# Optimization experiments

Hardware: AMD Instinct MI355X
Metric: run time of the kernel (lower is better)

## Reference

```python
import jax, jax.numpy as jnp
import numpy as np


def setup_inputs() -> dict:
    key = jax.random.key(0)
    k1, k2, k3 = jax.random.split(key, 3)
    B, D, G = 128, 1024, 40
    x = jax.random.normal(k1, (B, D), dtype=jnp.float32)
    g = jax.random.randint(k2, (B,), 0, 100, dtype=jnp.int64)
    layer_transform_0 = jax.random.normal(k3, (G, D, D), dtype=jnp.float32)
    return {"x": x, "g": g, "layer_transform_0": layer_transform_0, "l": 0, "n": 1}


def reference(x, g, layer_transform_0, l, n):
    # l selects which layer transform table; only one table here (layer_sizes=[1024]).
    # n is unused by the original forward.
    G = layer_transform_0.shape[0]
    shape = x.shape
    xf = x.reshape(shape[0], -1)               # (B, D)
    idx = g % G                                 # (B,)
    T = layer_transform_0[idx]                  # (B, D, D) gathered per-sample matrices
    out = jnp.einsum('bd,bde->be', xf, T)       # batched matvec (M=1 bmm)
    return out.reshape(shape)
```

## Files before the change

kernel.cpp:

```cpp
#include <hip/hip_runtime.h>


#define B_DIM   128
#define D_DIM   1024
#define G_DIM   40
#define DSPLIT  16
#define DCHUNK  (D_DIM / DSPLIT)
#define SMAX    8
#define THREADS 256

template <int USE_ATOMIC>
__global__ __launch_bounds__(THREADS) void leqfc_grouped(
    const float* __restrict__ x,
    const int* __restrict__ g,
    const float* __restrict__ T,
    float* __restrict__ part,
    float* __restrict__ out)
{
    const int gi  = blockIdx.x;
    const int dc  = blockIdx.y;
    const int dbase = dc * DCHUNK;
    const int tid = threadIdx.x;

    __shared__ int   mem[B_DIM];
    __shared__ int   cnt;
    __shared__ float xs[SMAX][DCHUNK];

    if (tid == 0) cnt = 0;
    __syncthreads();
    if (tid < B_DIM) {
        if ((g[tid] % G_DIM) == gi) {
            int i = atomicAdd(&cnt, 1);
            mem[i] = tid;
        }
    }
    __syncthreads();
    const int m = cnt;

    const float* __restrict__ Tg = T + (size_t)gi * D_DIM * D_DIM;
    const float4* __restrict__ Trow =
        reinterpret_cast<const float4*>(Tg + (size_t)dbase * D_DIM) + tid;

    for (int s0 = 0; s0 < m; s0 += SMAX) {
        const int mc = min(SMAX, m - s0);

        __syncthreads();
        #pragma unroll
        for (int k = 0; k < (SMAX * DCHUNK) / THREADS; ++k) {
            int idx = tid + k * THREADS;
            int j  = idx >> 6;
            int dd = idx & (DCHUNK - 1);
            xs[j][dd] = (j < mc)
                ? x[(size_t)mem[s0 + j] * D_DIM + dbase + dd]
                : 0.0f;
        }
        __syncthreads();

        float4 acc[SMAX];
        #pragma unroll
        for (int j = 0; j < SMAX; ++j) acc[j] = make_float4(0.f, 0.f, 0.f, 0.f);

        #pragma unroll 4
        for (int dd = 0; dd < DCHUNK; ++dd) {
            float4 t = Trow[(size_t)dd * (D_DIM / 4)];
            #pragma unroll
            for (int j = 0; j < SMAX; ++j) {
                float xv = xs[j][dd];
                acc[j].x = fmaf(xv, t.x, acc[j].x);
                acc[j].y = fmaf(xv, t.y, acc[j].y);
                acc[j].z = fmaf(xv, t.z, acc[j].z);
                acc[j].w = fmaf(xv, t.w, acc[j].w);
            }
        }

        #pragma unroll
        for (int j = 0; j < SMAX; ++j) {
            if (j < mc) {
                const int b = mem[s0 + j];
                if (USE_ATOMIC) {
                    float* o = out + (size_t)b * D_DIM + tid * 4;
                    atomicAdd(o + 0, acc[j].x);
                    atomicAdd(o + 1, acc[j].y);
                    atomicAdd(o + 2, acc[j].z);
                    atomicAdd(o + 3, acc[j].w);
                } else {
                    float4* o = reinterpret_cast<float4*>(
                        part + ((size_t)dc * B_DIM + b) * D_DIM) + tid;
                    *o = acc[j];
                }
            }
        }
    }
}

__global__ __launch_bounds__(256) void leqfc_reduce(
    const float* __restrict__ part, float* __restrict__ out)
{
    const int idx = blockIdx.x * 256 + threadIdx.x;
    float s = 0.f;
    #pragma unroll
    for (int p = 0; p < DSPLIT; ++p)
        s += part[(size_t)p * B_DIM * D_DIM + idx];
    out[idx] = s;
}

__global__ __launch_bounds__(256) void leqfc_zero(float* __restrict__ out)
{
    out[blockIdx.x * 256 + threadIdx.x] = 0.f;
}

extern "C" void kernel_launch(void* const* d_in, const int* in_sizes, int n_in,
                              void* d_out, int out_size, void* d_ws, size_t ws_size,
                              hipStream_t stream)
{
    const float* x = (const float*)d_in[0];
    const int*   g = (const int*)d_in[1];
    const float* T = (const float*)d_in[2];
    float* out = (float*)d_out;

    const size_t need = (size_t)DSPLIT * B_DIM * D_DIM * sizeof(float);
    dim3 grid(G_DIM, DSPLIT);

    if (ws_size >= need) {
        float* part = (float*)d_ws;
        leqfc_grouped<0><<<grid, THREADS, 0, stream>>>(x, g, T, part, nullptr);
        leqfc_reduce<<<(B_DIM * D_DIM) / 256, 256, 0, stream>>>(part, out);
    } else {
        leqfc_zero<<<(B_DIM * D_DIM) / 256, 256, 0, stream>>>(out);
        leqfc_grouped<1><<<grid, THREADS, 0, stream>>>(x, g, T, nullptr, out);
    }
}
```

Before: 33.40 us.

## Double the D split, prefetch T rows into registers, vectorize the reduction

```diff
diff --git a/kernel.cpp b/kernel.cpp
--- a/kernel.cpp
+++ b/kernel.cpp
@@ -4,10 +4,11 @@
 #define B_DIM   128
 #define D_DIM   1024
 #define G_DIM   40
-#define DSPLIT  16
+#define DSPLIT  32
 #define DCHUNK  (D_DIM / DSPLIT)
 #define SMAX    8
 #define THREADS 256
+#define PF      8
 
 template <int USE_ATOMIC>
 __global__ __launch_bounds__(THREADS) void leqfc_grouped(
@@ -17,10 +18,10 @@
     float* __restrict__ part,
     float* __restrict__ out)
 {
-    const int gi  = blockIdx.x;
-    const int dc  = blockIdx.y;
+    const int gi    = blockIdx.x;
+    const int dc    = blockIdx.y;
     const int dbase = dc * DCHUNK;
-    const int tid = threadIdx.x;
+    const int tid   = threadIdx.x;
 
     __shared__ int   mem[B_DIM];
     __shared__ int   cnt;
@@ -45,11 +46,9 @@
         const int mc = min(SMAX, m - s0);
 
         __syncthreads();
-        #pragma unroll
-        for (int k = 0; k < (SMAX * DCHUNK) / THREADS; ++k) {
-            int idx = tid + k * THREADS;
-            int j  = idx >> 6;
-            int dd = idx & (DCHUNK - 1);
+        {
+            int j  = tid >> 5;
+            int dd = tid & (DCHUNK - 1);
             xs[j][dd] = (j < mc)
                 ? x[(size_t)mem[s0 + j] * D_DIM + dbase + dd]
                 : 0.0f;
@@ -60,16 +59,27 @@
         #pragma unroll
         for (int j = 0; j < SMAX; ++j) acc[j] = make_float4(0.f, 0.f, 0.f, 0.f);
 
-        #pragma unroll 4
-        for (int dd = 0; dd < DCHUNK; ++dd) {
-            float4 t = Trow[(size_t)dd * (D_DIM / 4)];
+        float4 tbuf[PF];
+        #pragma unroll
+        for (int k = 0; k < PF; ++k)
+            tbuf[k] = Trow[(size_t)k * (D_DIM / 4)];
+
+        #pragma unroll
+        for (int dd0 = 0; dd0 < DCHUNK; dd0 += PF) {
             #pragma unroll
-            for (int j = 0; j < SMAX; ++j) {
-                float xv = xs[j][dd];
-                acc[j].x = fmaf(xv, t.x, acc[j].x);
-                acc[j].y = fmaf(xv, t.y, acc[j].y);
-                acc[j].z = fmaf(xv, t.z, acc[j].z);
-                acc[j].w = fmaf(xv, t.w, acc[j].w);
+            for (int k = 0; k < PF; ++k) {
+                float4 t = tbuf[k];
+                if (dd0 + PF + k < DCHUNK)
+                    tbuf[k] = Trow[(size_t)(dd0 + PF + k) * (D_DIM / 4)];
+                const int dd = dd0 + k;
+                #pragma unroll
+                for (int j = 0; j < SMAX; ++j) {
+                    const float xv = xs[j][dd];
+                    acc[j].x = fmaf(xv, t.x, acc[j].x);
+                    acc[j].y = fmaf(xv, t.y, acc[j].y);
+                    acc[j].z = fmaf(xv, t.z, acc[j].z);
+                    acc[j].w = fmaf(xv, t.w, acc[j].w);
+                }
             }
         }
 
@@ -97,11 +107,14 @@
     const float* __restrict__ part, float* __restrict__ out)
 {
     const int idx = blockIdx.x * 256 + threadIdx.x;
-    float s = 0.f;
+    const float4* p4 = reinterpret_cast<const float4*>(part);
+    float4 s = make_float4(0.f, 0.f, 0.f, 0.f);
     #pragma unroll
-    for (int p = 0; p < DSPLIT; ++p)
-        s += part[(size_t)p * B_DIM * D_DIM + idx];
-    out[idx] = s;
+    for (int p = 0; p < DSPLIT; ++p) {
+        float4 v = p4[(size_t)p * (B_DIM * D_DIM / 4) + idx];
+        s.x += v.x; s.y += v.y; s.z += v.z; s.w += v.w;
+    }
+    reinterpret_cast<float4*>(out)[idx] = s;
 }
 
 __global__ __launch_bounds__(256) void leqfc_zero(float* __restrict__ out)
@@ -124,7 +137,7 @@
     if (ws_size >= need) {
         float* part = (float*)d_ws;
         leqfc_grouped<0><<<grid, THREADS, 0, stream>>>(x, g, T, part, nullptr);
-        leqfc_reduce<<<(B_DIM * D_DIM) / 256, 256, 0, stream>>>(part, out);
+        leqfc_reduce<<<(B_DIM * D_DIM / 4) / 256, 256, 0, stream>>>(part, out);
     } else {
         leqfc_zero<<<(B_DIM * D_DIM) / 256, 256, 0, stream>>>(out);
         leqfc_grouped<1><<<grid, THREADS, 0, stream>>>(x, g, T, nullptr, out);
```

After: 41.86 us. 25.3% more time.
